# Kernel optimization log

Hardware: AMD Instinct MI355X
Metric: run time of the kernel (lower is better)

## Reference

```python
import jax, jax.numpy as jnp
import numpy as np

B, S, D, H = 4, 1024, 1024, 16
DH = D // H  # head dim = 64


def setup_inputs() -> dict:
    key = jax.random.key(0)
    k0, k1, k2 = jax.random.split(key, 3)
    x = jax.random.normal(k0, (B, S, D), dtype=jnp.float32)
    c_attn_w = jax.random.normal(k1, (D, 3 * D), dtype=jnp.float32) * 0.02
    c_attn_b = jnp.zeros((3 * D,), dtype=jnp.float32)
    c_proj_w = jax.random.normal(k2, (D, D), dtype=jnp.float32) * 0.02
    c_proj_b = jnp.zeros((D,), dtype=jnp.float32)
    return {"x": x, "c_attn_w": c_attn_w, "c_attn_b": c_attn_b,
            "c_proj_w": c_proj_w, "c_proj_b": c_proj_b}


def reference(x, c_attn_w, c_attn_b, c_proj_w, c_proj_b):
    b, s, d = x.shape
    # Conv1D (GPT-2 style): out = x @ W + b, fused QKV
    qkv = jnp.einsum('bsd,de->bse', x, c_attn_w) + c_attn_b
    q, k, v = jnp.split(qkv, 3, axis=-1)
    # split heads -> [b, h, s, dh]
    q = q.reshape(b, s, H, DH).transpose(0, 2, 1, 3)
    k = k.reshape(b, s, H, DH).transpose(0, 2, 1, 3)
    v = v.reshape(b, s, H, DH).transpose(0, 2, 1, 3)
    # scaled scores with causal future mask (triu above diagonal -> -inf)
    w = jnp.einsum('bhqd,bhkd->bhqk', q, k) / jnp.sqrt(jnp.asarray(DH, x.dtype))
    future = jnp.triu(jnp.ones((s, s), dtype=bool), k=1)
    w = jnp.where(future[None, None, :, :], jnp.asarray(-jnp.inf, w.dtype), w)
    p = jax.nn.softmax(w, axis=-1)
    a = jnp.einsum('bhqk,bhkd->bhqd', p, v)
    # merge heads -> [b, s, d]
    a = a.transpose(0, 2, 1, 3).reshape(b, s, d)
    # output projection (Conv1D)
    out = jnp.einsum('bsd,de->bse', a, c_proj_w) + c_proj_b
    return out
```

## Files before the change

### kernel.cpp

```cpp
#include <hip/hip_runtime.h>
#include <math.h>

#define BB 4
#define SS 1024
#define DD 1024
#define HH 16
#define DHH 64

typedef short bf16x8 __attribute__((ext_vector_type(8)));
typedef float f32x4 __attribute__((ext_vector_type(4)));

__device__ __forceinline__ unsigned short f2bf(float f) {
    unsigned u = __float_as_uint(f);
    u += 0x7fffu + ((u >> 16) & 1u);
    return (unsigned short)(u >> 16);
}

__device__ __forceinline__ void glds16(const void* g, void* l) {
    __builtin_amdgcn_global_load_lds(
        (const __attribute__((address_space(1))) unsigned int*)g,
        (__attribute__((address_space(3))) unsigned int*)l, 16, 0, 0);
}

#define WAITCNT_VM(n)  (0xF70 | (n))
#define WAITCNT_LGKM0  (0xC07F)

__device__ __forceinline__ int swz(int row, int col) {
    return ((((col >> 4) ^ (row >> 2)) & 3) << 4) | (col & 15);
}

#define XCD_REMAP(flat, NWG) (((flat) & 7) * ((NWG) >> 3) + ((flat) >> 3))

__global__ __launch_bounds__(256) void prologue_kernel(
    const float* __restrict__ x, const float* __restrict__ w1,
    const float* __restrict__ w2, unsigned short* __restrict__ Xb,
    unsigned short* __restrict__ W1t, unsigned short* __restrict__ W2t)
{
    __shared__ float tile[64][65];
    const int bx = blockIdx.x;
    if (bx < 4096) {
        int i = bx * 256 + threadIdx.x;
        float4 v = ((const float4*)x)[i];
        ushort4 o = { f2bf(v.x), f2bf(v.y), f2bf(v.z), f2bf(v.w) };
        ((ushort4*)Xb)[i] = o;
        return;
    }
    const float* W; unsigned short* Wt; int N, n0, k0;
    if (bx < 4864) {
        int id = bx - 4096; W = w1; Wt = W1t; N = 3072;
        n0 = (id % 48) * 64; k0 = (id / 48) * 64;
    } else {
        int id = bx - 4864; W = w2; Wt = W2t; N = 1024;
        n0 = (id & 15) * 64; k0 = (id >> 4) * 64;
    }
    int c = threadIdx.x & 63, r0 = threadIdx.x >> 6;
    #pragma unroll
    for (int i = 0; i < 16; ++i) {
        int r = r0 + i * 4;
        tile[r][c] = W[(size_t)(k0 + r) * N + n0 + c];
    }
    __syncthreads();
    #pragma unroll
    for (int i = 0; i < 16; ++i) {
        int r = r0 + i * 4;
        Wt[(size_t)(n0 + r) * 1024 + k0 + c] = f2bf(tile[c][r]);
    }
}

__global__ __launch_bounds__(512, 2) void gemm_mfma(
    const unsigned short* __restrict__ A,
    const unsigned short* __restrict__ Bt,
    const float* __restrict__ bias,
    unsigned short* __restrict__ Cout,
    unsigned short* __restrict__ Vt,
    int N, int K)
{
    __shared__ unsigned short smem[65536];

    const int t = threadIdx.x;
    const int lane = t & 63;
    const int w = t >> 6;
    const int l15 = lane & 15, quad = lane >> 4;
    const int wr = w >> 2, wc = w & 3;

    const int flat = XCD_REMAP(blockIdx.y * 16 + blockIdx.x, 256);
    const int tm = flat >> 4, tn = flat & 15;
    const int bm = tm * 256, bn = tn * 192;

    const int sl_ca  = ((lane & 7) ^ (lane >> 3)) << 4;
    const int sl_odd = (sl_ca >= 64);
    const int sl_k   = (sl_ca & 63) >> 1;
    const int lane_pr = w * 8 + (lane >> 3);

    const unsigned short* Asrc = A + (size_t)(bm + 2 * lane_pr + sl_odd) * K + sl_k;
    const unsigned short* Bsrc0 = Bt + (size_t)(bn + 2 * lane_pr + sl_odd) * K + sl_k;
    int brow1 = 128 + 2 * lane_pr + sl_odd;
    if (brow1 > 191) brow1 = 191;
    const unsigned short* Bsrc1 = Bt + (size_t)(bn + brow1) * K + sl_k;

    auto stageA = [&](int tile, int kh) {
        int toff = tile * 64 + kh * 32;
        int dst = ((tile & 1) * 2 + kh) * 16384;
        glds16(Asrc + toff,                    &smem[dst + w * 512]);
        glds16(Asrc + (size_t)128 * K + toff,  &smem[dst + 4096 + w * 512]);
    };
    auto stageB = [&](int tile, int kh) {
        int toff = tile * 64 + kh * 32;
        int dst = ((tile & 1) * 2 + kh) * 16384 + 8192;
        glds16(Bsrc0 + toff, &smem[dst + w * 512]);
        glds16(Bsrc1 + toff, &smem[dst + 4096 + w * 512]);
    };

    const f32x4 zero4 = {0.f, 0.f, 0.f, 0.f};
    f32x4 acc[8][3];
    #pragma unroll
    for (int i = 0; i < 8; ++i)
        #pragma unroll
        for (int j = 0; j < 3; ++j) acc[i][j] = zero4;

    const int T = K / 64;

    stageA(0, 0); stageB(0, 0); stageA(0, 1); stageB(0, 1);
    stageA(1, 0); stageB(1, 0);
    __builtin_amdgcn_s_waitcnt(WAITCNT_VM(4));

    bf16x8 bfr[3];
    for (int tt = 0; tt < T; ++tt) {
        const int buf = tt & 1;
        #pragma unroll
        for (int ph = 0; ph < 4; ++ph) {
            const int kh = ph >> 1;
            const int mh = ph & 1;
            __builtin_amdgcn_s_barrier();
            __builtin_amdgcn_sched_barrier(0);

            bf16x8 af[4];
            #pragma unroll
            for (int i = 0; i < 4; ++i) {
                int ar = wr * 128 + (mh * 4 + i) * 16 + l15;
                int byte = (ar >> 1) * 128 + (ar & 1) * 64 + (quad << 4);
                byte ^= ((ar >> 1) & 7) << 4;
                af[i] = *(const bf16x8*)&smem[(buf * 2 + kh) * 16384 + (byte >> 1)];
            }
            if (mh == 0) {
                #pragma unroll
                for (int nj = 0; nj < 3; ++nj) {
                    int br = wc * 48 + nj * 16 + l15;
                    int byte = 16384 + (br >> 1) * 128 + (br & 1) * 64 + (quad << 4);
                    byte ^= ((br >> 1) & 7) << 4;
                    bfr[nj] = *(const bf16x8*)&smem[(buf * 2 + kh) * 16384 + (byte >> 1)];
                }
            }

            if (ph == 0)      { if (tt + 1 < T) stageA(tt + 1, 1); }
            else if (ph == 1) { if (tt + 1 < T) stageB(tt + 1, 1); }
            else if (ph == 2) { if (tt + 2 < T) stageA(tt + 2, 0); }
            else              { if (tt + 2 < T) stageB(tt + 2, 0); }

            __builtin_amdgcn_s_setprio(1);
            #pragma unroll
            for (int i = 0; i < 4; ++i)
                #pragma unroll
                for (int nj = 0; nj < 3; ++nj)
                    acc[mh * 4 + i][nj] = __builtin_amdgcn_mfma_f32_16x16x32_bf16(
                        af[i], bfr[nj], acc[mh * 4 + i][nj], 0, 0, 0);
            __builtin_amdgcn_s_setprio(0);

            __builtin_amdgcn_s_barrier();
        }
        if (tt + 2 < T)      __builtin_amdgcn_s_waitcnt(WAITCNT_VM(4));
        else if (tt + 1 < T) __builtin_amdgcn_s_waitcnt(WAITCNT_VM(0));
    }

    __syncthreads();

    float bv[3];
    #pragma unroll
    for (int nj = 0; nj < 3; ++nj) bv[nj] = bias[bn + wc * 48 + nj * 16 + l15];

    const int b = bm >> 10, s0 = bm & 1023;

    if (tn <= 9) {
        #pragma unroll
        for (int mi = 0; mi < 8; ++mi)
            #pragma unroll
            for (int nj = 0; nj < 3; ++nj)
                #pragma unroll
                for (int r = 0; r < 4; ++r) {
                    int row = wr * 128 + mi * 16 + quad * 4 + r;
                    int col = wc * 48 + nj * 16 + l15;
                    smem[row * 192 + (col ^ (((row >> 2) & 3) << 4))] =
                        f2bf(acc[mi][nj][r] + bv[nj]);
                }
        __syncthreads();
        #pragma unroll
        for (int it = 0; it < 12; ++it) {
            int chunk = it * 512 + t;
            int row = chunk / 24;
            int col = (chunk % 24) * 8;
            bf16x8 val = *(const bf16x8*)&smem[row * 192 +
                         (col ^ (((row >> 2) & 3) << 4))];
            *(bf16x8*)&Cout[(size_t)(bm + row) * N + bn + col] = val;
        }
    } else if (tn >= 11) {
        #pragma unroll
        for (int mi = 0; mi < 8; ++mi)
            #pragma unroll
            for (int nj = 0; nj < 3; ++nj)
                #pragma unroll
                for (int r = 0; r < 4; ++r) {
                    int row = wr * 128 + mi * 16 + quad * 4 + r;
                    int col = wc * 48 + nj * 16 + l15;
                    smem[col * 256 + (row ^ (((col >> 2) & 3) << 4))] =
                        f2bf(acc[mi][nj][r] + bv[nj]);
                }
        __syncthreads();
        int h0 = (bn - 2048) >> 6;
        #pragma unroll
        for (int it = 0; it < 12; ++it) {
            int chunk = it * 512 + t;
            int col = chunk >> 5;
            int r8 = (chunk & 31) * 8;
            bf16x8 val = *(const bf16x8*)&smem[col * 256 +
                         (r8 ^ (((col >> 2) & 3) << 4))];
            int h = h0 + (col >> 6), dh = col & 63;
            *(bf16x8*)&Vt[(((size_t)b * 16 + h) * 64 + dh) * 1024 + s0 + r8] = val;
        }
    } else {
        #pragma unroll
        for (int mi = 0; mi < 8; ++mi)
            #pragma unroll
            for (int nj = 0; nj < 3; ++nj)
                #pragma unroll
                for (int r = 0; r < 4; ++r) {
                    int row = wr * 128 + mi * 16 + quad * 4 + r;
                    int col = wc * 48 + nj * 16 + l15;
                    unsigned short v = f2bf(acc[mi][nj][r] + bv[nj]);
                    if (col < 128)
                        smem[row * 128 + (col ^ (((row >> 2) & 3) << 4))] = v;
                    else {
                        int vc = col - 128;
                        smem[32768 + vc * 256 + (row ^ (((vc >> 2) & 3) << 4))] = v;
                    }
                }
        __syncthreads();
        #pragma unroll
        for (int it = 0; it < 8; ++it) {
            int chunk = it * 512 + t;
            int row = chunk >> 4;
            int col = (chunk & 15) * 8;
            bf16x8 val = *(const bf16x8*)&smem[row * 128 +
                         (col ^ (((row >> 2) & 3) << 4))];
            *(bf16x8*)&Cout[(size_t)(bm + row) * N + bn + col] = val;
        }
        #pragma unroll
        for (int it = 0; it < 4; ++it) {
            int chunk = it * 512 + t;
            int vc = chunk >> 5;
            int r8 = (chunk & 31) * 8;
            bf16x8 val = *(const bf16x8*)&smem[32768 + vc * 256 +
                         (r8 ^ (((vc >> 2) & 3) << 4))];
            *(bf16x8*)&Vt[(((size_t)b * 16 + 0) * 64 + vc) * 1024 + s0 + r8] = val;
        }
    }
}

__global__ __launch_bounds__(256) void gemm2_mfma(
    const unsigned short* __restrict__ A,
    const unsigned short* __restrict__ Bt,
    const float* __restrict__ bias,
    float* __restrict__ C,
    int N, int K)
{
    __shared__ unsigned short smem[18432];

    const int t = threadIdx.x;
    const int lane = t & 63;
    const int w = t >> 6;
    const int l15 = lane & 15, quad = lane >> 4;

    const int flat = XCD_REMAP(blockIdx.y * 8 + blockIdx.x, 512);
    const int bm = (flat / 8) * 64, bn = (flat % 8) * 128;

    const int fragoff = l15 * K + quad * 8;

    const f32x4 zero4 = {0.f, 0.f, 0.f, 0.f};
    f32x4 acc[2][4];
    #pragma unroll
    for (int i = 0; i < 2; ++i)
        #pragma unroll
        for (int j = 0; j < 4; ++j) acc[i][j] = zero4;

    const unsigned short* Abase = A  + (size_t)bm * K + fragoff;
    const unsigned short* Bbase = Bt + (size_t)bn * K + fragoff;

    const int R = K / 32;

    auto issue = [&](int k, int b) {
        glds16(Abase + (size_t)(w * 16) * K + k * 32,
               &smem[b * 6144 + w * 512]);
        #pragma unroll
        for (int g2 = 0; g2 < 2; ++g2) {
            int g = w * 2 + g2;
            glds16(Bbase + (size_t)(g * 16) * K + k * 32,
                   &smem[b * 6144 + 2048 + g * 512]);
        }
    };

    issue(0, 0);
    issue(1, 1);
    for (int k = 0; k < R; ++k) {
        if (k + 2 < R) {
            issue(k + 2, (k + 2) % 3);
            __builtin_amdgcn_s_waitcnt(WAITCNT_VM(6));
        } else if (k + 1 < R) {
            __builtin_amdgcn_s_waitcnt(WAITCNT_VM(3));
        } else {
            __builtin_amdgcn_s_waitcnt(WAITCNT_VM(0));
        }
        __builtin_amdgcn_s_barrier();

        bf16x8 af[2], bfr[4];
        #pragma unroll
        for (int mi = 0; mi < 2; ++mi)
            af[mi] = *(const bf16x8*)&smem[(k % 3) * 6144 + ((w >> 1) * 2 + mi) * 512 + lane * 8];
        #pragma unroll
        for (int nj = 0; nj < 4; ++nj)
            bfr[nj] = *(const bf16x8*)&smem[(k % 3) * 6144 + 2048 + ((w & 1) * 4 + nj) * 512 + lane * 8];
        #pragma unroll
        for (int mi = 0; mi < 2; ++mi)
            #pragma unroll
            for (int nj = 0; nj < 4; ++nj)
                acc[mi][nj] = __builtin_amdgcn_mfma_f32_16x16x32_bf16(
                    af[mi], bfr[nj], acc[mi][nj], 0, 0, 0);

        __builtin_amdgcn_s_barrier();
    }

    const int wm = (w >> 1) * 32;
    const int wn = (w & 1) * 64;
    float bv[4];
    #pragma unroll
    for (int nj = 0; nj < 4; ++nj) bv[nj] = bias[bn + wn + nj * 16 + l15];

    float* fs = (float*)smem;
    #pragma unroll
    for (int mi = 0; mi < 2; ++mi)
        #pragma unroll
        for (int nj = 0; nj < 4; ++nj)
            #pragma unroll
            for (int r = 0; r < 4; ++r)
                fs[(wm + mi * 16 + quad * 4 + r) * 128 + wn + nj * 16 + l15] =
                    acc[mi][nj][r] + bv[nj];
    __syncthreads();
    #pragma unroll
    for (int i = 0; i < 8; ++i) {
        int off = i * 256 + t;
        int row = off >> 5, col = (off & 31) * 4;
        *(float4*)&C[(size_t)(bm + row) * N + bn + col] =
            *(const float4*)&fs[row * 128 + col];
    }
}

__device__ __forceinline__ void attn_tile_step8(
    bf16x8 q0, bf16x8 q1, float* lsum, f32x4* o,
    const unsigned short (*Ks)[80], const unsigned short (*VsT)[80],
    unsigned short (*Ps)[80],
    int wq, int l15, int quad, bool diag)
{
    const f32x4 zero4 = {0.f, 0.f, 0.f, 0.f};
    f32x4 s[4];
    #pragma unroll
    for (int nj = 0; nj < 4; ++nj) {
        int n = nj * 16 + l15;
        f32x4 sa = zero4;
        bf16x8 b0 = *(const bf16x8*)&Ks[n][swz(n, quad * 8)];
        bf16x8 b1 = *(const bf16x8*)&Ks[n][swz(n, 32 + quad * 8)];
        sa = __builtin_amdgcn_mfma_f32_16x16x32_bf16(q0, b0, sa, 0, 0, 0);
        sa = __builtin_amdgcn_mfma_f32_16x16x32_bf16(q1, b1, sa, 0, 0, 0);
        s[nj] = sa;
    }
    const float scale = 0.125f;

    #pragma unroll
    for (int nj = 0; nj < 4; ++nj)
        #pragma unroll
        for (int r = 0; r < 4; ++r) {
            float sv = s[nj][r] * scale;
            if (diag && (nj * 16 + l15) > (wq * 16 + quad * 4 + r)) sv = -INFINITY;
            float p = __expf(sv);
            lsum[r] += p;
            int qloc = wq * 16 + quad * 4 + r;
            Ps[qloc][swz(qloc, nj * 16 + l15)] = f2bf(p);
        }

    #pragma unroll
    for (int kk = 0; kk < 2; ++kk) {
        int m = wq * 16 + l15;
        bf16x8 pa = *(const bf16x8*)&Ps[m][swz(m, kk * 32 + quad * 8)];
        #pragma unroll
        for (int nj = 0; nj < 4; ++nj) {
            int n = nj * 16 + l15;
            bf16x8 vb = *(const bf16x8*)&VsT[n][swz(n, kk * 32 + quad * 8)];
            o[nj] = __builtin_amdgcn_mfma_f32_16x16x32_bf16(pa, vb, o[nj], 0, 0, 0);
        }
    }
}

__global__ __launch_bounds__(512) void attn_mfma(
    const unsigned short* __restrict__ qkv,
    const unsigned short* __restrict__ Vt,
    unsigned short* __restrict__ aout)
{
    __shared__ unsigned short Ks[2][64][80];
    __shared__ unsigned short VsT[2][64][80];
    __shared__ unsigned short Ps[2][64][80];

    const int t = threadIdx.x;
    const int lane = t & 63;
    const int wave = t >> 6;
    const int wq = wave & 3;
    const int tile = wave >> 2;
    const int l15 = lane & 15, quad = lane >> 4;

    const int flat = XCD_REMAP(blockIdx.y * 8 + blockIdx.x, 512);
    const int qlo = flat % 8;
    const int bh = flat / 8;

    const int qhi = 15 - qlo;
    const int qb = tile ? qhi : qlo;
    const int b = bh >> 4, h = bh & 15;
    const size_t qkvbase = (size_t)b * SS * 3072;
    const f32x4 zero4 = {0.f, 0.f, 0.f, 0.f};

    bf16x8 qf0, qf1;
    {
        const unsigned short* p = qkv + qkvbase +
            (size_t)(qb * 64 + wq * 16 + l15) * 3072 + h * 64 + quad * 8;
        qf0 = *(const bf16x8*)p;
        qf1 = *(const bf16x8*)(p + 32);
    }

    float lsum[4];
    f32x4 o[4];
    #pragma unroll
    for (int r = 0; r < 4; ++r) lsum[r] = 0.f;
    #pragma unroll
    for (int nj = 0; nj < 4; ++nj) o[nj] = zero4;

    const int sr = t >> 3, scc = (t & 7) * 8;
    const unsigned short* kgp = qkv + qkvbase + 1024 + h * 64 + (size_t)sr * 3072 + scc;
    const unsigned short* vgp = Vt + ((size_t)bh * 64 + sr) * 1024 + scc;
    const int klds = swz(sr, scc);
    bf16x8 kreg, vreg;

    kreg = *(const bf16x8*)(kgp);
    vreg = *(const bf16x8*)(vgp);
    *(bf16x8*)&Ks[0][sr][klds] = kreg;
    *(bf16x8*)&VsT[0][sr][klds] = vreg;
    kreg = *(const bf16x8*)(kgp + (size_t)64 * 3072);
    vreg = *(const bf16x8*)(vgp + 64);
    __builtin_amdgcn_s_waitcnt(WAITCNT_LGKM0);
    __builtin_amdgcn_s_barrier();

    for (int kb = 0; kb <= qhi; ++kb) {
        const int cur = kb & 1;
        if (kb < qhi) {
            *(bf16x8*)&Ks[cur ^ 1][sr][klds] = kreg;
            *(bf16x8*)&VsT[cur ^ 1][sr][klds] = vreg;
            if (kb + 1 < qhi) {
                kreg = *(const bf16x8*)(kgp + (size_t)(kb + 2) * 64 * 3072);
                vreg = *(const bf16x8*)(vgp + (kb + 2) * 64);
            }
        }
        if (kb <= qb)
            attn_tile_step8(qf0, qf1, lsum, o, Ks[cur], VsT[cur], Ps[tile],
                            wq, l15, quad, kb == qb);
        __builtin_amdgcn_s_waitcnt(WAITCNT_LGKM0);
        __builtin_amdgcn_s_barrier();
    }

    #pragma unroll
    for (int off = 1; off < 16; off <<= 1)
        #pragma unroll
        for (int r = 0; r < 4; ++r)
            lsum[r] += __shfl_xor(lsum[r], off);

    #pragma unroll
    for (int r = 0; r < 4; ++r) {
        float inv = 1.0f / lsum[r];
        int rloc = wq * 16 + quad * 4 + r;
        size_t ob = ((size_t)b * SS + qb * 64 + rloc) * 1024 + h * 64;
        #pragma unroll
        for (int nj = 0; nj < 4; ++nj)
            aout[ob + nj * 16 + l15] = f2bf(o[nj][r] * inv);
    }
}

extern "C" void kernel_launch(void* const* d_in, const int* in_sizes, int n_in,
                              void* d_out, int out_size, void* d_ws, size_t ws_size,
                              hipStream_t stream)
{
    const float* x     = (const float*)d_in[0];
    const float* wqkv  = (const float*)d_in[1];
    const float* bqkv  = (const float*)d_in[2];
    const float* wproj = (const float*)d_in[3];
    const float* bproj = (const float*)d_in[4];
    float* out = (float*)d_out;

    unsigned short* ws   = (unsigned short*)d_ws;
    unsigned short* Xb   = ws;
    unsigned short* W1t  = Xb  + (size_t)4096 * 1024;
    unsigned short* W2t  = W1t + (size_t)3072 * 1024;
    unsigned short* qkv  = W2t + (size_t)1024 * 1024;
    unsigned short* Vt   = qkv + (size_t)4096 * 3072;
    unsigned short* abuf = Vt  + (size_t)64 * 64 * 1024;

    prologue_kernel<<<5120, 256, 0, stream>>>(x, wqkv, wproj, Xb, W1t, W2t);

    gemm_mfma<<<dim3(16, 16), 512, 0, stream>>>(
        Xb, W1t, bqkv, qkv, Vt, 3072, 1024);

    attn_mfma<<<dim3(8, 64), 512, 0, stream>>>(qkv, Vt, abuf);

    gemm2_mfma<<<dim3(1024 / 128, 4096 / 64), 256, 0, stream>>>(
        abuf, W2t, bproj, out, 1024, 1024);
}
```

Baseline: 163.4 us.

## Halve QKV GEMM M-tile to 128 rows and simplify staging pipeline

The QKV projection GEMM tile shrinks from 256x192 to 128x192, which doubles the grid to 512 blocks and cuts LDS to 80 KB so more blocks fit per CU (launch bounds raised to 4). The four-phase staggered prefetch becomes a two-phase double buffer: each k-half prefetches the next tile and then waits on a vmcnt before the barrier. The aim is better CU occupancy and load balance on the 256-CU part. The cost is lower per-block data reuse, so more global/L2 traffic per FLOP, and less room to hide latency within a block.

Measured after the change: 172.1 us. 5.3% more time.

```diff
diff --git a/kernel.cpp b/kernel.cpp
--- a/kernel.cpp
+++ b/kernel.cpp
@@ -67,7 +67,7 @@
     }
 }
 
-__global__ __launch_bounds__(512, 2) void gemm_mfma(
+__global__ __launch_bounds__(512, 4) void gemm_mfma(
     const unsigned short* __restrict__ A,
     const unsigned short* __restrict__ Bt,
     const float* __restrict__ bias,
@@ -75,7 +75,7 @@
     unsigned short* __restrict__ Vt,
     int N, int K)
 {
-    __shared__ unsigned short smem[65536];
+    __shared__ unsigned short smem[40960];
 
     const int t = threadIdx.x;
     const int lane = t & 63;
@@ -83,93 +83,87 @@
     const int l15 = lane & 15, quad = lane >> 4;
     const int wr = w >> 2, wc = w & 3;
 
-    const int flat = XCD_REMAP(blockIdx.y * 16 + blockIdx.x, 256);
+    const int flat = XCD_REMAP(blockIdx.y * 16 + blockIdx.x, 512);
     const int tm = flat >> 4, tn = flat & 15;
-    const int bm = tm * 256, bn = tn * 192;
+    const int bm = tm * 128, bn = tn * 192;
 
     const int sl_ca  = ((lane & 7) ^ (lane >> 3)) << 4;
     const int sl_odd = (sl_ca >= 64);
     const int sl_k   = (sl_ca & 63) >> 1;
-    const int lane_pr = w * 8 + (lane >> 3);
-
-    const unsigned short* Asrc = A + (size_t)(bm + 2 * lane_pr + sl_odd) * K + sl_k;
-    const unsigned short* Bsrc0 = Bt + (size_t)(bn + 2 * lane_pr + sl_odd) * K + sl_k;
-    int brow1 = 128 + 2 * lane_pr + sl_odd;
-    if (brow1 > 191) brow1 = 191;
-    const unsigned short* Bsrc1 = Bt + (size_t)(bn + brow1) * K + sl_k;
-
-    auto stageA = [&](int tile, int kh) {
-        int toff = tile * 64 + kh * 32;
-        int dst = ((tile & 1) * 2 + kh) * 16384;
-        glds16(Asrc + toff,                    &smem[dst + w * 512]);
-        glds16(Asrc + (size_t)128 * K + toff,  &smem[dst + 4096 + w * 512]);
+    const int pr  = w * 8 + (lane >> 3);
+    const int pr2 = (w < 4) ? pr : 0;
+
+    const unsigned short* Asrc  = A  + (size_t)(bm + 2 * pr  + sl_odd) * K + sl_k;
+    const unsigned short* Bsrc0 = Bt + (size_t)(bn + 2 * pr  + sl_odd) * K + sl_k;
+    const unsigned short* Bsrc1 = Bt + (size_t)(bn + 128 + 2 * pr2 + sl_odd) * K + sl_k;
+
+    auto stage = [&](int tile, int kh, int buf) {
+        const int toff = tile * 64 + kh * 32;
+        const int rb = (buf * 2 + kh) * 10240;
+        glds16(Asrc + toff,  &smem[rb + w * 512]);
+        glds16(Bsrc0 + toff, &smem[rb + 4096 + w * 512]);
+        if (w < 4)
+            glds16(Bsrc1 + toff, &smem[rb + 8192 + w * 512]);
     };
-    auto stageB = [&](int tile, int kh) {
-        int toff = tile * 64 + kh * 32;
-        int dst = ((tile & 1) * 2 + kh) * 16384 + 8192;
-        glds16(Bsrc0 + toff, &smem[dst + w * 512]);
-        glds16(Bsrc1 + toff, &smem[dst + 4096 + w * 512]);
-    };
 
     const f32x4 zero4 = {0.f, 0.f, 0.f, 0.f};
-    f32x4 acc[8][3];
-    #pragma unroll
-    for (int i = 0; i < 8; ++i)
+    f32x4 acc[4][3];
+    #pragma unroll
+    for (int i = 0; i < 4; ++i)
         #pragma unroll
         for (int j = 0; j < 3; ++j) acc[i][j] = zero4;
 
     const int T = K / 64;
 
-    stageA(0, 0); stageB(0, 0); stageA(0, 1); stageB(0, 1);
-    stageA(1, 0); stageB(1, 0);
-    __builtin_amdgcn_s_waitcnt(WAITCNT_VM(4));
-
-    bf16x8 bfr[3];
+    stage(0, 0, 0);
+    stage(0, 1, 0);
+    if (w < 4) __builtin_amdgcn_s_waitcnt(WAITCNT_VM(3));
+    else       __builtin_amdgcn_s_waitcnt(WAITCNT_VM(2));
+    __builtin_amdgcn_s_barrier();
+    __builtin_amdgcn_sched_barrier(0);
+
     for (int tt = 0; tt < T; ++tt) {
         const int buf = tt & 1;
         #pragma unroll
-        for (int ph = 0; ph < 4; ++ph) {
-            const int kh = ph >> 1;
-            const int mh = ph & 1;
-            __builtin_amdgcn_s_barrier();
-            __builtin_amdgcn_sched_barrier(0);
-
-            bf16x8 af[4];
+        for (int kh = 0; kh < 2; ++kh) {
+            const int rb = (buf * 2 + kh) * 10240;
+
+            bf16x8 af[4], bfr[3];
             #pragma unroll
             for (int i = 0; i < 4; ++i) {
-                int ar = wr * 128 + (mh * 4 + i) * 16 + l15;
+                int ar = wr * 64 + i * 16 + l15;
                 int byte = (ar >> 1) * 128 + (ar & 1) * 64 + (quad << 4);
                 byte ^= ((ar >> 1) & 7) << 4;
-                af[i] = *(const bf16x8*)&smem[(buf * 2 + kh) * 16384 + (byte >> 1)];
+                af[i] = *(const bf16x8*)&smem[rb + (byte >> 1)];
             }
-            if (mh == 0) {
-                #pragma unroll
-                for (int nj = 0; nj < 3; ++nj) {
-                    int br = wc * 48 + nj * 16 + l15;
-                    int byte = 16384 + (br >> 1) * 128 + (br & 1) * 64 + (quad << 4);
-                    byte ^= ((br >> 1) & 7) << 4;
-                    bfr[nj] = *(const bf16x8*)&smem[(buf * 2 + kh) * 16384 + (byte >> 1)];
-                }
+            #pragma unroll
+            for (int nj = 0; nj < 3; ++nj) {
+                int br = wc * 48 + nj * 16 + l15;
+                int byte = (br >> 1) * 128 + (br & 1) * 64 + (quad << 4);
+                byte ^= ((br >> 1) & 7) << 4;
+                bfr[nj] = *(const bf16x8*)&smem[rb + 4096 + (byte >> 1)];
             }
 
-            if (ph == 0)      { if (tt + 1 < T) stageA(tt + 1, 1); }
-            else if (ph == 1) { if (tt + 1 < T) stageB(tt + 1, 1); }
-            else if (ph == 2) { if (tt + 2 < T) stageA(tt + 2, 0); }
-            else              { if (tt + 2 < T) stageB(tt + 2, 0); }
+            if (tt + 1 < T) stage(tt + 1, kh, buf ^ 1);
 
             __builtin_amdgcn_s_setprio(1);
             #pragma unroll
             for (int i = 0; i < 4; ++i)
                 #pragma unroll
                 for (int nj = 0; nj < 3; ++nj)
-                    acc[mh * 4 + i][nj] = __builtin_amdgcn_mfma_f32_16x16x32_bf16(
-                        af[i], bfr[nj], acc[mh * 4 + i][nj], 0, 0, 0);
+                    acc[i][nj] = __builtin_amdgcn_mfma_f32_16x16x32_bf16(
+                        af[i], bfr[nj], acc[i][nj], 0, 0, 0);
             __builtin_amdgcn_s_setprio(0);
 
+            if (tt + 1 < T) {
+                if (w < 4) __builtin_amdgcn_s_waitcnt(WAITCNT_VM(3));
+                else       __builtin_amdgcn_s_waitcnt(WAITCNT_VM(2));
+            } else {
+                __builtin_amdgcn_s_waitcnt(WAITCNT_VM(0));
+            }
             __builtin_amdgcn_s_barrier();
-        }
-        if (tt + 2 < T)      __builtin_amdgcn_s_waitcnt(WAITCNT_VM(4));
-        else if (tt + 1 < T) __builtin_amdgcn_s_waitcnt(WAITCNT_VM(0));
+            __builtin_amdgcn_sched_barrier(0);
+        }
     }
 
     __syncthreads();
@@ -182,19 +176,19 @@
 
     if (tn <= 9) {
         #pragma unroll
-        for (int mi = 0; mi < 8; ++mi)
+        for (int mi = 0; mi < 4; ++mi)
             #pragma unroll
             for (int nj = 0; nj < 3; ++nj)
                 #pragma unroll
                 for (int r = 0; r < 4; ++r) {
-                    int row = wr * 128 + mi * 16 + quad * 4 + r;
+                    int row = wr * 64 + mi * 16 + quad * 4 + r;
                     int col = wc * 48 + nj * 16 + l15;
                     smem[row * 192 + (col ^ (((row >> 2) & 3) << 4))] =
                         f2bf(acc[mi][nj][r] + bv[nj]);
                 }
         __syncthreads();
         #pragma unroll
-        for (int it = 0; it < 12; ++it) {
+        for (int it = 0; it < 6; ++it) {
             int chunk = it * 512 + t;
             int row = chunk / 24;
             int col = (chunk % 24) * 8;
@@ -204,48 +198,48 @@
         }
     } else if (tn >= 11) {
         #pragma unroll
-        for (int mi = 0; mi < 8; ++mi)
+        for (int mi = 0; mi < 4; ++mi)
             #pragma unroll
             for (int nj = 0; nj < 3; ++nj)
                 #pragma unroll
                 for (int r = 0; r < 4; ++r) {
-                    int row = wr * 128 + mi * 16 + quad * 4 + r;
+                    int row = wr * 64 + mi * 16 + quad * 4 + r;
                     int col = wc * 48 + nj * 16 + l15;
-                    smem[col * 256 + (row ^ (((col >> 2) & 3) << 4))] =
+                    smem[col * 128 + (row ^ (((col >> 2) & 3) << 4))] =
                         f2bf(acc[mi][nj][r] + bv[nj]);
                 }
         __syncthreads();
         int h0 = (bn - 2048) >> 6;
         #pragma unroll
-        for (int it = 0; it < 12; ++it) {
+        for (int it = 0; it < 6; ++it) {
             int chunk = it * 512 + t;
-            int col = chunk >> 5;
-            int r8 = (chunk & 31) * 8;
-            bf16x8 val = *(const bf16x8*)&smem[col * 256 +
+            int col = chunk >> 4;
+            int r8 = (chunk & 15) * 8;
+            bf16x8 val = *(const bf16x8*)&smem[col * 128 +
                          (r8 ^ (((col >> 2) & 3) << 4))];
             int h = h0 + (col >> 6), dh = col & 63;
             *(bf16x8*)&Vt[(((size_t)b * 16 + h) * 64 + dh) * 1024 + s0 + r8] = val;
         }
     } else {
         #pragma unroll
-        for (int mi = 0; mi < 8; ++mi)
+        for (int mi = 0; mi < 4; ++mi)
             #pragma unroll
             for (int nj = 0; nj < 3; ++nj)
                 #pragma unroll
                 for (int r = 0; r < 4; ++r) {
-                    int row = wr * 128 + mi * 16 + quad * 4 + r;
+                    int row = wr * 64 + mi * 16 + quad * 4 + r;
                     int col = wc * 48 + nj * 16 + l15;
                     unsigned short v = f2bf(acc[mi][nj][r] + bv[nj]);
                     if (col < 128)
                         smem[row * 128 + (col ^ (((row >> 2) & 3) << 4))] = v;
                     else {
                         int vc = col - 128;
-                        smem[32768 + vc * 256 + (row ^ (((vc >> 2) & 3) << 4))] = v;
+                        smem[16384 + vc * 128 + (row ^ (((vc >> 2) & 3) << 4))] = v;
                     }
                 }
         __syncthreads();
         #pragma unroll
-        for (int it = 0; it < 8; ++it) {
+        for (int it = 0; it < 4; ++it) {
             int chunk = it * 512 + t;
             int row = chunk >> 4;
             int col = (chunk & 15) * 8;
@@ -254,11 +248,11 @@
             *(bf16x8*)&Cout[(size_t)(bm + row) * N + bn + col] = val;
         }
         #pragma unroll
-        for (int it = 0; it < 4; ++it) {
+        for (int it = 0; it < 2; ++it) {
             int chunk = it * 512 + t;
-            int vc = chunk >> 5;
-            int r8 = (chunk & 31) * 8;
-            bf16x8 val = *(const bf16x8*)&smem[32768 + vc * 256 +
+            int vc = chunk >> 4;
+            int r8 = (chunk & 15) * 8;
+            bf16x8 val = *(const bf16x8*)&smem[16384 + vc * 128 +
                          (r8 ^ (((vc >> 2) & 3) << 4))];
             *(bf16x8*)&Vt[(((size_t)b * 16 + 0) * 64 + vc) * 1024 + s0 + r8] = val;
         }
@@ -518,7 +512,7 @@
 
     prologue_kernel<<<5120, 256, 0, stream>>>(x, wqkv, wproj, Xb, W1t, W2t);
 
-    gemm_mfma<<<dim3(16, 16), 512, 0, stream>>>(
+    gemm_mfma<<<dim3(16, 32), 512, 0, stream>>>(
         Xb, W1t, bqkv, qkv, Vt, 3072, 1024);
 
     attn_mfma<<<dim3(8, 64), 512, 0, stream>>>(qkv, Vt, abuf);
```
